# Kernel tuning notes

Hardware: AMD Instinct MI355X
Metric: run time of the kernel (lower is better)

## Reference

```python
import jax, jax.numpy as jnp
import numpy as np

B, V, LP, LO = 256, 128000, 1024, 256


def setup_inputs() -> dict:
    key = jax.random.key(0)
    ks = jax.random.split(key, 11)
    logits = jax.random.normal(ks[0], (B, V), jnp.float32) * 4.0
    presence_penalties = jax.random.uniform(ks[1], (B,), jnp.float32, 0.0, 0.5)
    frequency_penalties = jax.random.uniform(ks[2], (B,), jnp.float32, 0.0, 0.5)
    repetition_penalties = jax.random.uniform(ks[3], (B,), jnp.float32, 1.0, 1.3)
    temperatures = jax.random.uniform(ks[4], (B,), jnp.float32, 0.5, 1.5)
    top_ps = jax.random.uniform(ks[5], (B,), jnp.float32, 0.8, 1.0)
    top_as = jax.random.uniform(ks[6], (B,), jnp.float32, 0.0, 0.2)
    min_ps = jax.random.uniform(ks[7], (B,), jnp.float32, 0.0, 0.1)
    prompt_tokens = jax.random.randint(ks[8], (B, LP), 0, V, jnp.int32)
    output_tokens = jax.random.randint(ks[9], (B, LO), 0, V, jnp.int32)
    top_ks = jax.random.randint(ks[10], (B,), 1, 2048, jnp.int32)
    return dict(logits=logits, presence_penalties=presence_penalties,
                frequency_penalties=frequency_penalties,
                repetition_penalties=repetition_penalties,
                temperatures=temperatures, top_ps=top_ps, top_as=top_as,
                min_ps=min_ps, prompt_tokens=prompt_tokens,
                output_tokens=output_tokens, top_ks=top_ks)


def _bin_counts(tokens, num_seqs, vocab):
    # scatter-add histogram of token ids per row (torch _get_bin_counts_and_mask)
    rows = jnp.arange(num_seqs)[:, None]
    counts = jnp.zeros((num_seqs, vocab), jnp.int32).at[rows, tokens].add(1)
    return counts, counts > 0


def reference(logits, presence_penalties, frequency_penalties,
              repetition_penalties, temperatures, top_ps, top_as, min_ps,
              prompt_tokens, output_tokens, top_ks):
    num_seqs, vocab = logits.shape

    # ---- _apply_penalties ----
    _, prompt_mask = _bin_counts(prompt_tokens, num_seqs, vocab)
    out_counts, out_mask = _bin_counts(output_tokens, num_seqs, vocab)
    rep = jnp.where(prompt_mask | out_mask, repetition_penalties[:, None], 1.0)
    logits = jnp.where(logits > 0, logits / rep, logits * rep)
    logits = logits - frequency_penalties[:, None] * out_counts.astype(logits.dtype)
    logits = logits - presence_penalties[:, None] * out_mask.astype(logits.dtype)

    # ---- _apply_temperature (static path; dynatemp mins/maxs == 0) ----
    temps = jnp.where(temperatures == 0.0, 1.0, temperatures)
    logits = logits / temps[:, None]

    # ---- _apply_alphabet_soup: top-p / top-k / top-a / min-p ----
    order = jnp.argsort(-logits, axis=-1)               # descending sort order
    logits_sort = jnp.take_along_axis(logits, order, axis=-1)
    probs_sort = jax.nn.softmax(logits_sort, axis=-1)
    probs_sum = jnp.cumsum(probs_sort, axis=-1) - probs_sort  # exclusive cumsum
    p_top = probs_sort[:, :1]
    threshold = jnp.maximum(p_top * min_ps[:, None],
                            (p_top * p_top) * top_as[:, None])
    mask = (probs_sort < threshold) | (probs_sum > top_ps[:, None])
    mask = mask.at[:, 0].set(False)                     # always keep argmax
    mask = mask | (jnp.arange(vocab)[None, :] >= top_ks[:, None])  # per-row top-k
    logits_sort = jnp.where(mask, -jnp.inf, logits_sort)

    inv = jnp.argsort(order, axis=-1)                   # inverse permutation
    return jnp.take_along_axis(logits_sort, inv, axis=-1)
```

## Files before the change

kernel.cpp:

```cpp
#include <hip/hip_runtime.h>
#include <hip/hip_fp16.h>
#include <cstdint>

#define NV 128000
#define NROWS 256
#define NLP 1024
#define NLO 256
#define HASH_SZ 4096
#define HEMPTY 0xFFFFFFFFu
#define NBINS 2048
#define TBIN 1216
#define GCAP 4096
#define M0 40.0f
#define LOG2E 1.44269504f
#define MASK16 0xFBFFu
#define MASK32 0xFBFFFBFFu

#define HIST_BYTES (NROWS * NBINS * 4)
#define WS_ZERO_BYTES (HIST_BYTES + NROWS * 4)

__device__ __forceinline__ int lbin(float l) {
    int b = (int)((l + 32.0f) * 32.0f);
    return max(0, min(b, NBINS - 1));
}

__device__ __forceinline__ float dec_bf16(uint32_t b) {
    union { uint32_t u; float f; } c; c.u = b << 16; return c.f;
}
__device__ __forceinline__ float dec_fp16(uint32_t h) {
    uint32_t s = h >> 15, e = (h >> 10) & 31u, m = h & 1023u;
    union { uint32_t u; float f; } c;
    if (e == 0) { c.u = (s << 31) | (103u << 23); return c.f * (float)m; }
    if (e == 31) return s ? -65504.0f : 65504.0f;
    c.u = (s << 31) | ((e + 112u) << 23) | (m << 13);
    return c.f;
}
__device__ __forceinline__ float ldf(const void* p, size_t i, int mode) {
    if (mode == 0) return ((const float*)p)[i];
    uint32_t h = ((const unsigned short*)p)[i];
    return (mode == 1) ? dec_bf16(h) : dec_fp16(h);
}
__device__ __forceinline__ uint32_t enc_fp16_safe(float r) {
    if (!(r == r)) r = 0.0f;
    if (r >  65504.0f) r =  65504.0f;
    if (r < -65504.0f) r = -65504.0f;
    uint32_t b = __half_as_ushort(__float2half(r));
    if ((b & 0x7C00u) == 0x7C00u) b = (b & 0x8000u) ? MASK16 : 0x7BFFu;
    return b;
}
__device__ __forceinline__ int sniff_mode(const void* logits) {
    const unsigned short* w = (const unsigned short*)logits;
    int bf = 0, fp = 0;
    for (int i = 0; i < 128; ++i) {
        uint32_t h = w[i];
        uint32_t e8 = (h >> 7) & 0xFFu;
        uint32_t e5 = (h >> 10) & 0x1Fu;
        if (e8 >= 110 && e8 <= 142) bf++;
        if (e5 >= 8 && e5 <= 22) fp++;
    }
    return (bf >= 109) ? 1 : ((fp >= 109) ? 2 : 0);
}

__device__ __forceinline__ void hash_insert(uint32_t* keys, uint32_t* vals,
                                            uint32_t token, uint32_t addv, uint32_t orv) {
    uint32_t h = (token * 2654435761u) & (HASH_SZ - 1);
    while (true) {
        uint32_t k = keys[h];
        if (k == token) break;
        if (k == HEMPTY) {
            uint32_t old = atomicCAS(&keys[h], HEMPTY, token);
            if (old == HEMPTY || old == token) break;
        }
        h = (h + 1) & (HASH_SZ - 1);
    }
    if (addv) atomicAdd(&vals[h], addv);
    if (orv)  atomicOr(&vals[h], orv);
}
__device__ __forceinline__ bool hash_contains(const uint32_t* keys, uint32_t token) {
    uint32_t h = (token * 2654435761u) & (HASH_SZ - 1);
    while (true) {
        uint32_t k = keys[h];
        if (k == token) return true;
        if (k == HEMPTY) return false;
        h = (h + 1) & (HASH_SZ - 1);
    }
}

__device__ __forceinline__ float blk_sum(float v, float* red, int tid) {
    #pragma unroll
    for (int o = 32; o > 0; o >>= 1) v += __shfl_down(v, o, 64);
    __syncthreads();
    if ((tid & 63) == 0) red[tid >> 6] = v;
    __syncthreads();
    if (tid < 64) {
        float w = (tid < 16) ? red[tid] : 0.0f;
        #pragma unroll
        for (int o = 8; o > 0; o >>= 1) w += __shfl_down(w, o, 64);
        if (tid == 0) red[0] = w;
    }
    __syncthreads();
    return red[0];
}
__device__ __forceinline__ int blk_imin(int v, int* red, int tid) {
    #pragma unroll
    for (int o = 32; o > 0; o >>= 1) v = min(v, __shfl_down(v, o, 64));
    __syncthreads();
    if ((tid & 63) == 0) red[tid >> 6] = v;
    __syncthreads();
    if (tid < 64) {
        int w = (tid < 16) ? red[tid] : 0x7FFFFFFF;
        #pragma unroll
        for (int o = 8; o > 0; o >>= 1) w = min(w, __shfl_down(w, o, 64));
        if (tid == 0) red[0] = w;
    }
    __syncthreads();
    return red[0];
}

__device__ __forceinline__ void gappend(bool pred, float x, int idx,
                                        int* gcnt, float* g_x, int* g_i, int lane) {
    unsigned long long mask = __ballot(pred);
    if (mask == 0ull) return;
    int cnt = __popcll(mask);
    int ldr = __ffsll((unsigned long long)mask) - 1;
    int base = 0;
    if (lane == ldr) base = atomicAdd(gcnt, cnt);
    base = __shfl(base, ldr, 64);
    if (pred) {
        int pos = base + __popcll(mask & ((1ull << lane) - 1ull));
        if (pos < GCAP) { g_x[pos] = x; g_i[pos] = idx; }
    }
}

__global__ __launch_bounds__(256) void k1_hist_z(
    const void* __restrict__ logits,
    const void* __restrict__ temperature,
    uint32_t* __restrict__ hist,
    float* __restrict__ zrow)
{
    const int row  = blockIdx.x >> 2;
    const int part = blockIdx.x & 3;
    const int tid  = threadIdx.x;

    __shared__ uint32_t sh[NBINS];
    __shared__ float sred[4];
    __shared__ int s_mode;
    if (tid == 0) s_mode = sniff_mode(logits);
    for (int i = tid; i < NBINS; i += 256) sh[i] = 0u;
    __syncthreads();
    const int mode = s_mode;

    float temp = ldf(temperature, row, mode);
    if (temp == 0.0f) temp = 1.0f;
    const float c1 = (1.0f / temp) * LOG2E;
    const float c0 = -M0 * LOG2E;

    float zs = 0.0f;
    const int base = part * 32000;
    if (mode == 0) {
        const float4* l4 = (const float4*)((const float*)logits + (size_t)row * NV + base);
        for (int i = tid; i < 8000; i += 256) {
            float4 f = l4[i];
            int b0 = lbin(f.x), b1 = lbin(f.y), b2 = lbin(f.z), b3 = lbin(f.w);
            zs += exp2f(fmaf(f.x, c1, c0)); if (b0 >= TBIN) atomicAdd(&sh[b0], 1u);
            zs += exp2f(fmaf(f.y, c1, c0)); if (b1 >= TBIN) atomicAdd(&sh[b1], 1u);
            zs += exp2f(fmaf(f.z, c1, c0)); if (b2 >= TBIN) atomicAdd(&sh[b2], 1u);
            zs += exp2f(fmaf(f.w, c1, c0)); if (b3 >= TBIN) atomicAdd(&sh[b3], 1u);
        }
    } else {
        for (int i = tid; i < 32000; i += 256) {
            float l = ldf(logits, (size_t)row * NV + base + i, mode);
            int b = lbin(l);
            zs += exp2f(fmaf(l, c1, c0));
            if (b >= TBIN) atomicAdd(&sh[b], 1u);
        }
    }
    #pragma unroll
    for (int o = 32; o > 0; o >>= 1) zs += __shfl_down(zs, o, 64);
    __syncthreads();
    if ((tid & 63) == 0) sred[tid >> 6] = zs;
    __syncthreads();
    if (tid == 0) atomicAdd(&zrow[row], sred[0] + sred[1] + sred[2] + sred[3]);

    uint32_t* gh = hist + (size_t)row * NBINS;
    for (int j = TBIN + tid; j < NBINS; j += 256) {
        uint32_t s = sh[j];
        if (s) atomicAdd(&gh[j], s);
    }
}

__global__ __launch_bounds__(1024) void k2_select(
    const void* __restrict__ logits,
    const void* __restrict__ presence,
    const void* __restrict__ frequency,
    const void* __restrict__ repetition,
    const void* __restrict__ temperature,
    const void* __restrict__ top_ps,
    const void* __restrict__ top_as,
    const void* __restrict__ min_ps,
    const int*  __restrict__ prompt_tokens,
    const int*  __restrict__ output_tokens,
    const int*  __restrict__ top_ks,
    const uint32_t* __restrict__ hist,
    const float* __restrict__ zrow,
    unsigned short* __restrict__ out)
{
    const int row  = blockIdx.x;
    const int tid  = threadIdx.x;
    const int lane = tid & 63;
    const int wid  = tid >> 6;

    __shared__ uint32_t hkey[HASH_SZ];
    __shared__ uint32_t hval[HASH_SZ];
    __shared__ float    g_x[GCAP];
    __shared__ int      g_i[GCAP];
    __shared__ uint32_t sS[NBINS];
    __shared__ float red[16];
    __shared__ uint32_t uws[16], uoff[16];
    __shared__ float    fws[16], foff[16];
    __shared__ int s_mode, s_bstar, s_gcnt, s_nkeep;

    if (tid == 0) { s_mode = sniff_mode(logits); s_gcnt = 0; s_bstar = TBIN; }
    for (int i = tid; i < HASH_SZ; i += 1024) { hkey[i] = HEMPTY; hval[i] = 0u; }
    {
        const uint32_t* gh = hist + (size_t)row * NBINS;
        for (int j = tid; j < NBINS; j += 1024) sS[j] = gh[NBINS - 1 - j];
    }
    __syncthreads();
    const int mode = s_mode;

    {
        const int* ot = output_tokens + row * NLO;
        for (int i = tid; i < NLO; i += 1024)
            hash_insert(hkey, hval, (uint32_t)ot[i], 1u, 0u);
        const int* pt = prompt_tokens + row * NLP;
        for (int i = tid; i < NLP; i += 1024)
            hash_insert(hkey, hval, (uint32_t)pt[i], 0u, 0x10000u);
    }
    __syncthreads();

    const float rep  = ldf(repetition, row, mode);
    const float freq = ldf(frequency, row, mode);
    const float pres = ldf(presence, row, mode);
    float temp = ldf(temperature, row, mode);
    if (temp == 0.0f) temp = 1.0f;
    const float tinv = 1.0f / temp;

    float zd = 0.0f;
    for (int s = tid; s < HASH_SZ; s += 1024) {
        uint32_t k = hkey[s];
        if (k != HEMPTY) {
            float l = ldf(logits, (size_t)row * NV + k, mode);
            uint32_t v = hval[s];
            float pl = (l > 0.0f) ? (l / rep) : (l * rep);
            uint32_t cnt = v & 0xFFFFu;
            if (cnt) pl = pl - freq * (float)cnt - pres;
            int bo = lbin(l), bn = lbin(pl);
            if (bo != bn) {
                if (bo >= TBIN) atomicSub(&sS[NBINS - 1 - bo], 1u);
                if (bn >= TBIN) atomicAdd(&sS[NBINS - 1 - bn], 1u);
            }
            zd += __expf(pl * tinv - M0) - __expf(l * tinv - M0);
            hval[s] = __float_as_uint(pl);
        }
    }
    const float Z = zrow[row] + blk_sum(zd, red, tid);
    const float invZ = 1.0f / Z;

    int K = top_ks[row];
    if (K < 1) K = 1;
    if (K > 2047) K = 2047;

    {
        uint32_t v0 = sS[2 * tid], v1 = sS[2 * tid + 1];
        uint32_t s = v0 + v1;
        #pragma unroll
        for (int o = 1; o < 64; o <<= 1) {
            uint32_t t = __shfl_up(s, o, 64);
            if (lane >= o) s += t;
        }
        if (lane == 63) uws[wid] = s;
        __syncthreads();
        if (tid < 16) {
            uint32_t w = uws[tid];
            #pragma unroll
            for (int o = 1; o < 16; o <<= 1) {
                uint32_t t = __shfl_up(w, o, 64);
                if (tid >= o) w += t;
            }
            uoff[tid] = w - uws[tid];
        }
        __syncthreads();
        uint32_t incl1 = uoff[wid] + s;
        uint32_t incl0 = incl1 - v1;
        uint32_t prev0 = incl0 - v0;
        uint32_t Ku = (uint32_t)K;
        if (incl0 >= Ku && (tid == 0 || prev0 < Ku)) s_bstar = NBINS - 1 - 2 * tid;
        if (incl1 >= Ku && incl0 < Ku)               s_bstar = NBINS - 1 - (2 * tid + 1);
    }
    __syncthreads();
    const int bstar = s_bstar;

    unsigned short* orow = out + (size_t)row * NV;
    {
        uint4 sv; sv.x = MASK32; sv.y = MASK32; sv.z = MASK32; sv.w = MASK32;
        uint4* o4 = (uint4*)orow;
        for (int i = tid; i < 16000; i += 1024) o4[i] = sv;
    }

    if (mode == 0) {
        const float4* l4 = (const float4*)((const float*)logits + (size_t)row * NV);
        for (int i = tid; i < NV / 4; i += 1024) {
            float4 f = l4[i];
            int base = i * 4;
            #define GA(val, idx) {                                                     \
                bool pred = (lbin(val) >= bstar) && !hash_contains(hkey, (uint32_t)(idx)); \
                gappend(pred, (val) * tinv, (idx), &s_gcnt, g_x, g_i, lane); }
            GA(f.x, base + 0) GA(f.y, base + 1) GA(f.z, base + 2) GA(f.w, base + 3)
            #undef GA
        }
    } else {
        for (int i = tid; i < NV; i += 1024) {
            float l = ldf(logits, (size_t)row * NV + i, mode);
            bool pred = (lbin(l) >= bstar) && !hash_contains(hkey, (uint32_t)i);
            gappend(pred, l * tinv, i, &s_gcnt, g_x, g_i, lane);
        }
    }
    for (int s = tid; s < HASH_SZ; s += 1024) {
        uint32_t k = hkey[s];
        bool pred = (k != HEMPTY);
        float pl = 0.0f;
        if (pred) {
            pl = __uint_as_float(hval[s]);
            pred = (lbin(pl) >= bstar);
        }
        gappend(pred, pl * tinv, (int)k, &s_gcnt, g_x, g_i, lane);
    }
    __syncthreads();

    const int ng = min(s_gcnt, GCAP);
    int sn = 64; while (sn < ng) sn <<= 1;
    const int sortn = sn;
    const int padend = (sortn > 2048) ? GCAP : 2048;
    for (int i = ng + tid; i < padend; i += 1024) { g_x[i] = -INFINITY; g_i[i] = 0x7FFFFFFF; }
    __syncthreads();

    for (int k = 2; k <= sortn; k <<= 1) {
        for (int j = k >> 1; j > 0; j >>= 1) {
            if (j >= 64) __syncthreads();
            for (int p = tid; p < (sortn >> 1); p += 1024) {
                int i0 = 2 * p - (p & (j - 1));
                int i1 = i0 + j;
                bool up = ((i0 & k) == 0);
                float xa = g_x[i0], xb = g_x[i1];
                int ia = g_i[i0], ib = g_i[i1];
                bool aFirst = (xa > xb) || (xa == xb && ia < ib);
                if (aFirst != up) {
                    g_x[i0] = xb; g_x[i1] = xa;
                    g_i[i0] = ib; g_i[i1] = ia;
                }
            }
        }
    }
    __syncthreads();

    const float p0 = __expf(g_x[0] - M0) * invZ;
    const float thr = fmaxf(p0 * ldf(min_ps, row, mode),
                            p0 * p0 * ldf(top_as, row, mode));
    const float topp = ldf(top_ps, row, mode);

    float q0 = __expf(g_x[2 * tid]     - M0) * invZ;
    float q1 = __expf(g_x[2 * tid + 1] - M0) * invZ;
    float fs = q0 + q1;
    #pragma unroll
    for (int o = 1; o < 64; o <<= 1) {
        float t = __shfl_up(fs, o, 64);
        if (lane >= o) fs += t;
    }
    if (lane == 63) fws[wid] = fs;
    __syncthreads();
    if (tid < 16) {
        float w = fws[tid];
        #pragma unroll
        for (int o = 1; o < 16; o <<= 1) {
            float t = __shfl_up(w, o, 64);
            if (tid >= o) w += t;
        }
        foff[tid] = w - fws[tid];
    }
    __syncthreads();
    float incl1 = foff[wid] + fs;
    float cs1   = incl1 - q1;
    float cs0   = cs1 - q0;
    int fmv = 0x7FFFFFFF;
    if (tid > 0 && (q0 < thr || cs0 > topp)) fmv = 2 * tid;
    else if (q1 < thr || cs1 > topp)         fmv = 2 * tid + 1;
    const int fm = blk_imin(fmv, (int*)red, tid);
    if (tid == 0) {
        int nk = min(fm, K);
        if (nk < 1) nk = 1;
        s_nkeep = min(nk, ng);
    }
    __syncthreads();

    {
        const int nk = s_nkeep;
        for (int r = tid; r < nk; r += 1024)
            orow[g_i[r]] = (unsigned short)enc_fp16_safe(g_x[r]);
    }
}

extern "C" void kernel_launch(void* const* d_in, const int* in_sizes, int n_in,
                              void* d_out, int out_size, void* d_ws, size_t ws_size,
                              hipStream_t stream) {
    uint32_t* hist = (uint32_t*)d_ws;
    float* zrow = (float*)((char*)d_ws + HIST_BYTES);

    hipMemsetAsync(d_ws, 0, WS_ZERO_BYTES, stream);

    k1_hist_z<<<NROWS * 4, 256, 0, stream>>>(d_in[0], d_in[4], hist, zrow);

    k2_select<<<NROWS, 1024, 0, stream>>>(
        d_in[0], d_in[1], d_in[2], d_in[3], d_in[4], d_in[5], d_in[6], d_in[7],
        (const int*)d_in[8], (const int*)d_in[9], (const int*)d_in[10],
        hist, zrow, (unsigned short*)d_out);
}
```

Measured before the change: 362.1 us.

## Collect high-logit candidate indices in first pass, skip second full logits scan

The first kernel now appends the indices of logits above a fixed level to a per-row global candidate list instead of building a shared-memory histogram. It also takes over the masked-output fill and uses twice as many blocks per row. The select kernel then builds its histogram and gathers only from the candidate list plus the penalty hash table, avoiding a second full read of the logits row. The risks are global-atomic contention on the candidate counter, and correctness that depends on enough logits exceeding the fixed level to cover top-k, with at most 6144 candidates per row.

```diff
diff --git a/kernel.cpp b/kernel.cpp
--- a/kernel.cpp
+++ b/kernel.cpp
@@ -9,15 +9,20 @@
 #define HASH_SZ 4096
 #define HEMPTY 0xFFFFFFFFu
 #define NBINS 2048
-#define TBIN 1216
+#define TBIN 1262
+#define TLVL 7.4375f
+#define RBINS 1024
+#define GG 6144
 #define GCAP 4096
 #define M0 40.0f
 #define LOG2E 1.44269504f
 #define MASK16 0xFBFFu
 #define MASK32 0xFBFFFBFFu
 
-#define HIST_BYTES (NROWS * NBINS * 4)
-#define WS_ZERO_BYTES (HIST_BYTES + NROWS * 4)
+#define ZROW_OFF 0
+#define GCNT_OFF (NROWS * 4)
+#define CAND_OFF (2 * NROWS * 4)
+#define WS_ZERO_BYTES (2 * NROWS * 4)
 
 __device__ __forceinline__ int lbin(float l) {
     int b = (int)((l + 32.0f) * 32.0f);
@@ -132,21 +137,36 @@
     }
 }
 
-__global__ __launch_bounds__(256) void k1_hist_z(
+__device__ __forceinline__ void iappend_g(bool pred, uint32_t idx,
+                                          uint32_t* cnt, uint32_t* list, int lane) {
+    unsigned long long mask = __ballot(pred);
+    if (mask == 0ull) return;
+    int c = __popcll(mask);
+    int ldr = __ffsll((unsigned long long)mask) - 1;
+    int base = 0;
+    if (lane == ldr) base = (int)atomicAdd(cnt, (uint32_t)c);
+    base = __shfl(base, ldr, 64);
+    if (pred) {
+        int pos = base + __popcll(mask & ((1ull << lane) - 1ull));
+        if (pos < GG) list[pos] = idx;
+    }
+}
+
+__global__ __launch_bounds__(256) void k1_main(
     const void* __restrict__ logits,
     const void* __restrict__ temperature,
-    uint32_t* __restrict__ hist,
-    float* __restrict__ zrow)
+    float* __restrict__ zrow,
+    uint32_t* __restrict__ gcnt,
+    uint32_t* __restrict__ cand,
+    unsigned short* __restrict__ out)
 {
-    const int row  = blockIdx.x >> 2;
-    const int part = blockIdx.x & 3;
+    const int row  = blockIdx.x >> 3;
+    const int part = blockIdx.x & 7;
     const int tid  = threadIdx.x;
-
-    __shared__ uint32_t sh[NBINS];
-    __shared__ float sred[4];
+    const int lane = tid & 63;
+
     __shared__ int s_mode;
     if (tid == 0) s_mode = sniff_mode(logits);
-    for (int i = tid; i < NBINS; i += 256) sh[i] = 0u;
     __syncthreads();
     const int mode = s_mode;
 
@@ -155,38 +175,38 @@
     const float c1 = (1.0f / temp) * LOG2E;
     const float c0 = -M0 * LOG2E;
 
+    {
+        uint4 sv; sv.x = MASK32; sv.y = MASK32; sv.z = MASK32; sv.w = MASK32;
+        uint4* o4 = (uint4*)(out + (size_t)row * NV) + part * 2000;
+        for (int i = tid; i < 2000; i += 256) o4[i] = sv;
+    }
+
+    uint32_t* my_gcnt = gcnt + row;
+    uint32_t* my_cand = cand + (size_t)row * GG;
+
     float zs = 0.0f;
-    const int base = part * 32000;
+    const int base = part * 16000;
     if (mode == 0) {
         const float4* l4 = (const float4*)((const float*)logits + (size_t)row * NV + base);
-        for (int i = tid; i < 8000; i += 256) {
+        for (int i = tid; i < 4000; i += 256) {
             float4 f = l4[i];
-            int b0 = lbin(f.x), b1 = lbin(f.y), b2 = lbin(f.z), b3 = lbin(f.w);
-            zs += exp2f(fmaf(f.x, c1, c0)); if (b0 >= TBIN) atomicAdd(&sh[b0], 1u);
-            zs += exp2f(fmaf(f.y, c1, c0)); if (b1 >= TBIN) atomicAdd(&sh[b1], 1u);
-            zs += exp2f(fmaf(f.z, c1, c0)); if (b2 >= TBIN) atomicAdd(&sh[b2], 1u);
-            zs += exp2f(fmaf(f.w, c1, c0)); if (b3 >= TBIN) atomicAdd(&sh[b3], 1u);
+            int idx = base + i * 4;
+            #define KE(val, id) {                                         \
+                zs += exp2f(fmaf((val), c1, c0));                         \
+                iappend_g((val) >= TLVL, (uint32_t)(id), my_gcnt, my_cand, lane); }
+            KE(f.x, idx + 0) KE(f.y, idx + 1) KE(f.z, idx + 2) KE(f.w, idx + 3)
+            #undef KE
         }
     } else {
-        for (int i = tid; i < 32000; i += 256) {
+        for (int i = tid; i < 16000; i += 256) {
             float l = ldf(logits, (size_t)row * NV + base + i, mode);
-            int b = lbin(l);
             zs += exp2f(fmaf(l, c1, c0));
-            if (b >= TBIN) atomicAdd(&sh[b], 1u);
+            iappend_g(l >= TLVL, (uint32_t)(base + i), my_gcnt, my_cand, lane);
         }
     }
     #pragma unroll
     for (int o = 32; o > 0; o >>= 1) zs += __shfl_down(zs, o, 64);
-    __syncthreads();
-    if ((tid & 63) == 0) sred[tid >> 6] = zs;
-    __syncthreads();
-    if (tid == 0) atomicAdd(&zrow[row], sred[0] + sred[1] + sred[2] + sred[3]);
-
-    uint32_t* gh = hist + (size_t)row * NBINS;
-    for (int j = TBIN + tid; j < NBINS; j += 256) {
-        uint32_t s = sh[j];
-        if (s) atomicAdd(&gh[j], s);
-    }
+    if (lane == 0) atomicAdd(&zrow[row], zs);
 }
 
 __global__ __launch_bounds__(1024) void k2_select(
@@ -201,8 +221,9 @@
     const int*  __restrict__ prompt_tokens,
     const int*  __restrict__ output_tokens,
     const int*  __restrict__ top_ks,
-    const uint32_t* __restrict__ hist,
     const float* __restrict__ zrow,
+    const uint32_t* __restrict__ gcnt,
+    const uint32_t* __restrict__ cand,
     unsigned short* __restrict__ out)
 {
     const int row  = blockIdx.x;
@@ -214,7 +235,7 @@
     __shared__ uint32_t hval[HASH_SZ];
     __shared__ float    g_x[GCAP];
     __shared__ int      g_i[GCAP];
-    __shared__ uint32_t sS[NBINS];
+    __shared__ uint32_t sS[RBINS];
     __shared__ float red[16];
     __shared__ uint32_t uws[16], uoff[16];
     __shared__ float    fws[16], foff[16];
@@ -222,12 +243,22 @@
 
     if (tid == 0) { s_mode = sniff_mode(logits); s_gcnt = 0; s_bstar = TBIN; }
     for (int i = tid; i < HASH_SZ; i += 1024) { hkey[i] = HEMPTY; hval[i] = 0u; }
-    {
-        const uint32_t* gh = hist + (size_t)row * NBINS;
-        for (int j = tid; j < NBINS; j += 1024) sS[j] = gh[NBINS - 1 - j];
-    }
+    sS[tid] = 0u;
     __syncthreads();
     const int mode = s_mode;
+
+    const int ncand = min((int)gcnt[row], GG);
+    const uint32_t* cand_row = cand + (size_t)row * GG;
+    uint32_t ci[6]; float cl[6];
+    #pragma unroll
+    for (int k = 0; k < 6; ++k) {
+        int i = tid + k * 1024;
+        bool v = (i < ncand);
+        uint32_t id = v ? cand_row[i] : 0u;
+        float l = v ? ldf(logits, (size_t)row * NV + id, mode) : 0.0f;
+        ci[k] = id; cl[k] = l;
+        if (v) atomicAdd(&sS[NBINS - 1 - lbin(l)], 1u);
+    }
 
     {
         const int* ot = output_tokens + row * NLO;
@@ -272,8 +303,8 @@
     if (K > 2047) K = 2047;
 
     {
-        uint32_t v0 = sS[2 * tid], v1 = sS[2 * tid + 1];
-        uint32_t s = v0 + v1;
+        uint32_t v = sS[tid];
+        uint32_t s = v;
         #pragma unroll
         for (int o = 1; o < 64; o <<= 1) {
             uint32_t t = __shfl_up(s, o, 64);
@@ -291,40 +322,19 @@
             uoff[tid] = w - uws[tid];
         }
         __syncthreads();
-        uint32_t incl1 = uoff[wid] + s;
-        uint32_t incl0 = incl1 - v1;
-        uint32_t prev0 = incl0 - v0;
+        uint32_t incl = uoff[wid] + s;
+        uint32_t prev = incl - v;
         uint32_t Ku = (uint32_t)K;
-        if (incl0 >= Ku && (tid == 0 || prev0 < Ku)) s_bstar = NBINS - 1 - 2 * tid;
-        if (incl1 >= Ku && incl0 < Ku)               s_bstar = NBINS - 1 - (2 * tid + 1);
+        if (incl >= Ku && prev < Ku) s_bstar = NBINS - 1 - tid;
     }
     __syncthreads();
     const int bstar = s_bstar;
 
-    unsigned short* orow = out + (size_t)row * NV;
-    {
-        uint4 sv; sv.x = MASK32; sv.y = MASK32; sv.z = MASK32; sv.w = MASK32;
-        uint4* o4 = (uint4*)orow;
-        for (int i = tid; i < 16000; i += 1024) o4[i] = sv;
-    }
-
-    if (mode == 0) {
-        const float4* l4 = (const float4*)((const float*)logits + (size_t)row * NV);
-        for (int i = tid; i < NV / 4; i += 1024) {
-            float4 f = l4[i];
-            int base = i * 4;
-            #define GA(val, idx) {                                                     \
-                bool pred = (lbin(val) >= bstar) && !hash_contains(hkey, (uint32_t)(idx)); \
-                gappend(pred, (val) * tinv, (idx), &s_gcnt, g_x, g_i, lane); }
-            GA(f.x, base + 0) GA(f.y, base + 1) GA(f.z, base + 2) GA(f.w, base + 3)
-            #undef GA
-        }
-    } else {
-        for (int i = tid; i < NV; i += 1024) {
-            float l = ldf(logits, (size_t)row * NV + i, mode);
-            bool pred = (lbin(l) >= bstar) && !hash_contains(hkey, (uint32_t)i);
-            gappend(pred, l * tinv, i, &s_gcnt, g_x, g_i, lane);
-        }
+    #pragma unroll
+    for (int k = 0; k < 6; ++k) {
+        int i = tid + k * 1024;
+        bool pred = (i < ncand) && (lbin(cl[k]) >= bstar) && !hash_contains(hkey, ci[k]);
+        gappend(pred, cl[k] * tinv, (int)ci[k], &s_gcnt, g_x, g_i, lane);
     }
     for (int s = tid; s < HASH_SZ; s += 1024) {
         uint32_t k = hkey[s];
@@ -403,6 +413,7 @@
     }
     __syncthreads();
 
+    unsigned short* orow = out + (size_t)row * NV;
     {
         const int nk = s_nkeep;
         for (int r = tid; r < nk; r += 1024)
@@ -413,15 +424,18 @@
 extern "C" void kernel_launch(void* const* d_in, const int* in_sizes, int n_in,
                               void* d_out, int out_size, void* d_ws, size_t ws_size,
                               hipStream_t stream) {
-    uint32_t* hist = (uint32_t*)d_ws;
-    float* zrow = (float*)((char*)d_ws + HIST_BYTES);
+    char* ws = (char*)d_ws;
+    float*    zrow = (float*)(ws + ZROW_OFF);
+    uint32_t* gcnt = (uint32_t*)(ws + GCNT_OFF);
+    uint32_t* cand = (uint32_t*)(ws + CAND_OFF);
 
     hipMemsetAsync(d_ws, 0, WS_ZERO_BYTES, stream);
 
-    k1_hist_z<<<NROWS * 4, 256, 0, stream>>>(d_in[0], d_in[4], hist, zrow);
+    k1_main<<<NROWS * 8, 256, 0, stream>>>(
+        d_in[0], d_in[4], zrow, gcnt, cand, (unsigned short*)d_out);
 
     k2_select<<<NROWS, 1024, 0, stream>>>(
         d_in[0], d_in[1], d_in[2], d_in[3], d_in[4], d_in[5], d_in[6], d_in[7],
         (const int*)d_in[8], (const int*)d_in[9], (const int*)d_in[10],
-        hist, zrow, (unsigned short*)d_out);
-}
+        zrow, gcnt, cand, (unsigned short*)d_out);
+}
```

After: 842.0 us. 2.33x slower.
